# Optimization experiments

Measured on AMD Instinct MI355X. Metric: run time of the kernel, lower is better.

## Reference

```python
import jax, jax.numpy as jnp
import numpy as np

N = 50000  # nodes
E = 1600000  # edges
L = 2  # layers
D = 128  # input/hidden dim


def setup_inputs() -> dict:
    key = jax.random.key(0)
    ks = jax.random.split(key, 8)
    s = 1.0 / np.sqrt(D)
    return {
        "x": jax.random.normal(ks[0], (N, D), jnp.float32),
        "edge_index": jax.random.randint(ks[1], (2, E), 0, N, jnp.int64),
        "h": jax.random.normal(ks[2], (L, N, D), jnp.float32),
        "Wx": jax.random.normal(ks[3], (L, 3, D, D), jnp.float32) * s,
        "bx": jax.random.normal(ks[4], (L, 3, D), jnp.float32) * 0.01,
        "Wh": jax.random.normal(ks[5], (L, 3, D, D), jnp.float32) * s,
        "bh": jax.random.normal(ks[6], (L, 3, D), jnp.float32) * 0.01,
    }


def _gcn(x, W, b, src, dst, dinv):
    # GCNConv with added self-loops and symmetric normalization:
    # out = D^{-1/2} (A + I) D^{-1/2} X W + b
    hw = x @ W                                   # [N, H]
    norm = dinv[src] * dinv[dst]                 # [E]
    msg = hw[src] * norm[:, None]                # [E, H]
    agg = jax.ops.segment_sum(msg, dst, num_segments=N)
    agg = agg + hw * (dinv * dinv)[:, None]      # self-loop contribution
    return agg + b


def reference(x, edge_index, h, Wx, bx, Wh, bh):
    src = edge_index[0]
    dst = edge_index[1]
    # in-degree on destination nodes, including self-loop (+1)
    deg = jax.ops.segment_sum(jnp.ones((E,), x.dtype), dst, num_segments=N) + 1.0
    dinv = jax.lax.rsqrt(deg)

    outs = []
    inp = x
    for l in range(L):
        hl = h[l]
        z = jax.nn.sigmoid(_gcn(inp, Wx[l, 0], bx[l, 0], src, dst, dinv)
                           + _gcn(hl, Wh[l, 0], bh[l, 0], src, dst, dinv))
        r = jax.nn.sigmoid(_gcn(inp, Wx[l, 1], bx[l, 1], src, dst, dinv)
                           + _gcn(hl, Wh[l, 1], bh[l, 1], src, dst, dinv))
        h_tilde = jnp.tanh(_gcn(inp, Wx[l, 2], bx[l, 2], src, dst, dinv)
                           + _gcn(r * hl, Wh[l, 2], bh[l, 2], src, dst, dinv))
        out = z * hl + (1.0 - z) * h_tilde
        outs.append(out)
        inp = out
    return jnp.stack(outs, axis=0)  # [L, N, H]
```

## Files before the change

kernel.cpp:

```cpp
#include <hip/hip_runtime.h>

typedef __attribute__((ext_vector_type(8))) unsigned short us8;
typedef __attribute__((ext_vector_type(4))) unsigned short us4;
typedef __attribute__((ext_vector_type(8))) short s8;
typedef __attribute__((ext_vector_type(4))) float f4;
typedef __attribute__((ext_vector_type(2))) float f2;

#define DEV static __device__ __forceinline__
#define CAP 128
#define NRG 128
#define NBB 256
#define SEGC 128

DEV float bf2f(unsigned short h){ return __uint_as_float(((unsigned)h)<<16); }
DEV unsigned short f2bf(float f){
  unsigned x = __float_as_uint(f);
  x += 0x7fffu + ((x>>16)&1u);
  return (unsigned short)(x>>16);
}
DEV float sigm(float x){ return 1.f/(1.f + __expf(-x)); }

__global__ __launch_bounds__(256) void k_bucket(const int* __restrict__ src,
    const int* __restrict__ dst, unsigned* __restrict__ buf,
    int* __restrict__ cnt2, int e, int n){
  __shared__ int lcnt[NRG];
  int b = blockIdx.x;
  for(int i=threadIdx.x;i<NRG;i+=256) lcnt[i] = 0;
  __syncthreads();
  int chunk = (e + NBB - 1)/NBB;
  int lo = b*chunk;
  int hi = lo + chunk; if(hi>e) hi=e;
  for(int i = lo + threadIdx.x; i < hi; i += 256){
    int d = dst[i], s = src[i];
    int r = (d*NRG)/n;
    int pos = atomicAdd(&lcnt[r], 1);
    if(pos < SEGC)
      buf[((size_t)r*NBB + b)*SEGC + pos] = ((unsigned)d<<16) | (unsigned)s;
  }
  __syncthreads();
  for(int i=threadIdx.x;i<NRG;i+=256) cnt2[i*NBB + b] = lcnt[i];
}

__global__ __launch_bounds__(256) void k_build2(const unsigned* __restrict__ buf,
    const int* __restrict__ cnt2, int* __restrict__ cnt,
    unsigned short* __restrict__ col, int n){
  int r = blockIdx.x;
  int lo = (r*n + NRG-1)/NRG;
  int hi = ((r+1)*n + NRG-1)/NRG;
  int span = hi - lo;
  __shared__ int lc[512];
  for(int i=threadIdx.x; i<span; i+=256) lc[i] = 0;
  __syncthreads();
  int lane = threadIdx.x & 63;
  for(int seg = threadIdx.x>>6; seg < NBB; seg += 4){
    int c = cnt2[r*NBB + seg]; if(c > SEGC) c = SEGC;
    const unsigned* p = buf + ((size_t)r*NBB + seg)*SEGC;
    for(int i = lane; i < c; i += 64){
      unsigned v = p[i];
      int d = (int)(v >> 16), s = (int)(v & 0xffffu);
      int slot = atomicAdd(&lc[d - lo], 1);
      col[(size_t)d*CAP + slot] = (unsigned short)s;
    }
  }
  __syncthreads();
  for(int i=threadIdx.x; i<span; i+=256) cnt[lo + i] = lc[i];
}

__global__ void k_setup(const int* __restrict__ cnt, float* __restrict__ dinv, int n,
                        const float* __restrict__ Wx, const float* __restrict__ Wh,
                        unsigned short* __restrict__ WT,
                        const float* __restrict__ h, unsigned short* __restrict__ hb,
                        int htotal){
  int gN = (n + 255)/256;
  int b = blockIdx.x;
  if(b < gN){
    int i = b*256 + threadIdx.x;
    if(i<n) dinv[i] = rsqrtf((float)cnt[i] + 1.0f);
  } else if(b < gN + 768){
    int i = (b-gN)*256 + threadIdx.x;
    int m = i >> 15;
    int rem = i & 32767;
    int j = rem >> 8;
    int k = rem & 255;
    float v = (k<128) ? Wx[((size_t)m*128 + k)*128 + j]
                      : Wh[((size_t)m*128 + (k-128))*128 + j];
    WT[(size_t)m*32768 + j*256 + k] = f2bf(v);
  } else {
    size_t i = ((size_t)(b - gN - 768)*256 + threadIdx.x)*4;
    if(i < (size_t)htotal){
      f4 v = *(const f4*)(h + i);
      us4 w;
      #pragma unroll
      for(int j=0;j<4;++j) w[j] = f2bf(v[j]);
      *(us4*)(hb + i) = w;
    }
  }
}

__global__ void k_scale2(const float* __restrict__ inp, const unsigned short* __restrict__ hb0,
                         const float* __restrict__ dinv, unsigned char* __restrict__ y2, int n){
  int i = blockIdx.x*blockDim.x+threadIdx.x;
  if(i >= n*32) return;
  int node = i>>5, d0 = (i&31)*4;
  float dv = dinv[node];
  f4 a = *(const f4*)(inp + (size_t)node*128 + d0);
  us4 hv = *(const us4*)(hb0 + (size_t)node*128 + d0);
  unsigned pa = __builtin_amdgcn_cvt_pk_fp8_f32(dv*a[0], dv*a[1], 0, false);
  pa = __builtin_amdgcn_cvt_pk_fp8_f32(dv*a[2], dv*a[3], pa, true);
  unsigned pb = __builtin_amdgcn_cvt_pk_fp8_f32(dv*bf2f(hv[0]), dv*bf2f(hv[1]), 0, false);
  pb = __builtin_amdgcn_cvt_pk_fp8_f32(dv*bf2f(hv[2]), dv*bf2f(hv[3]), pb, true);
  *(unsigned*)(y2 + (size_t)node*256 + d0)       = pa;
  *(unsigned*)(y2 + (size_t)node*256 + 128 + d0) = pb;
}

template<int DB>
__global__ __launch_bounds__(256) void k_agg(const unsigned char* __restrict__ y,
    const int* __restrict__ cnt, const unsigned short* __restrict__ col,
    const float* __restrict__ dinv, unsigned short* __restrict__ out0, int n)
{
  constexpr int GL = DB/16;
  constexpr int NG = 64/GL;
  constexpr int U = 8;
  int tid = threadIdx.x;
  int wave = tid>>6, lane = tid&63;
  int g = lane/GL, gl = lane%GL;
  int node = blockIdx.x*(4*NG) + wave*NG + g;
  if(node >= n) return;
  const unsigned char* yb = y + (size_t)gl*16;
  float acc[16];
  {
    uint4 q = *(const uint4*)(yb + (size_t)node*DB);
    const unsigned* qw = (const unsigned*)&q;
    #pragma unroll
    for(int w=0;w<4;++w){
      f2 lo = __builtin_amdgcn_cvt_pk_f32_fp8(qw[w], false);
      f2 hi = __builtin_amdgcn_cvt_pk_f32_fp8(qw[w], true);
      acc[w*4+0]=lo[0]; acc[w*4+1]=lo[1]; acc[w*4+2]=hi[0]; acc[w*4+3]=hi[1];
    }
  }
  const unsigned short* myrow = col + (size_t)node*CAP;
  int c_ = cnt[node];
  int last = c_ - 1;
  for(int i=0; i<c_; i += U){
    int s[U];
    #pragma unroll
    for(int u=0;u<U;++u){
      int ii = i + u; ii = (ii < last) ? ii : last;
      s[u] = myrow[ii];
    }
    uint4 v[U];
    #pragma unroll
    for(int u=0;u<U;++u) v[u] = *(const uint4*)(yb + (size_t)s[u]*DB);
    #pragma unroll
    for(int u=0;u<U;++u){
      if(i + u < c_){
        const unsigned* qw = (const unsigned*)&v[u];
        #pragma unroll
        for(int w=0;w<4;++w){
          f2 lo = __builtin_amdgcn_cvt_pk_f32_fp8(qw[w], false);
          f2 hi = __builtin_amdgcn_cvt_pk_f32_fp8(qw[w], true);
          acc[w*4+0]+=lo[0]; acc[w*4+1]+=lo[1]; acc[w*4+2]+=hi[0]; acc[w*4+3]+=hi[1];
        }
      }
    }
  }
  float dv = dinv[node];
  us8 w0, w1;
  #pragma unroll
  for(int j=0;j<8;++j){ w0[j]=f2bf(acc[j]*dv); w1[j]=f2bf(acc[8+j]*dv); }
  int c = gl*16;
  *(us8*)(out0 + (size_t)node*DB + c)     = w0;
  *(us8*)(out0 + (size_t)node*DB + c + 8) = w1;
}

template<int KB>
DEV void stageB512(unsigned char* Bs, const unsigned short* Bsrc, int srcOff, int t){
  constexpr int CPR = KB/8;
  #pragma unroll
  for(int i=0;i<128*CPR/512;++i){
    int c = t + i*512;
    int j = c / CPR, kc = c % CPR;
    us8 v = *(const us8*)(Bsrc + (size_t)j*256 + srcOff + kc*8);
    *(us8*)(Bs + ((j*(KB*2) + kc*16) ^ ((j&7)<<4))) = v;
  }
}
template<int NK>
DEV void loadB(const unsigned short* A, int astride, int node, int nrows, int hi,
               s8 (&b)[NK]){
  const unsigned short* Ap = A + (size_t)(node < nrows ? node : 0)*astride + hi*8;
  #pragma unroll
  for(int kk=0;kk<NK;++kk) b[kk] = *(const s8*)(Ap + kk*32);
}
template<int KB, int NK, int NA>
DEV void mfmaW(const unsigned char* Bs, const s8 (&b)[NA], int lo, int hi,
               f4 (&acc)[8]){
  static_assert(NK <= NA, "not enough B fragments");
  #pragma unroll
  for(int kk=0;kk<NK;++kk){
    #pragma unroll
    for(int n=0;n<8;++n){
      int j = n*16+lo;
      s8 a = *(const s8*)(Bs + ((j*(KB*2) + kk*64 + hi*16) ^ ((lo&7)<<4)));
      acc[n] = __builtin_amdgcn_mfma_f32_16x16x32_bf16(a, b[kk], acc[n], 0,0,0);
    }
  }
}

__global__ __launch_bounds__(512) void k_gemmRH(
    const unsigned short* __restrict__ axah, const unsigned short* __restrict__ Wr,
    const unsigned short* __restrict__ Wh2, const unsigned short* __restrict__ hbl,
    const float* __restrict__ dinv, const float* __restrict__ bxr,
    const float* __restrict__ bhr, unsigned char* __restrict__ yq,
    unsigned short* __restrict__ Zbh, int nrows)
{
  __shared__ unsigned char Bs[65536];
  const int t = threadIdx.x, lane = t & 63, lo = lane & 15, hi = lane >> 4;
  const int node = blockIdx.x*128 + (t>>6)*16 + lo;
  const bool ok = node < nrows;
  s8 b256[8];
  loadB<8>(axah, 256, node, nrows, hi, b256);
  stageB512<256>(Bs, Wr, 0, t);
  f4 acc[8];
  #pragma unroll
  for(int n=0;n<8;++n) acc[n]=(f4)0.f;
  __syncthreads();
  mfmaW<256,8,8>(Bs, b256, lo, hi, acc);
  if(ok){
    float dv = dinv[node];
    const size_t base = (size_t)node*128;
    #pragma unroll
    for(int n=0;n<8;++n){
      int j0 = n*16 + hi*4;
      f4 b1v = *(const f4*)(bxr + j0);
      f4 b2v = *(const f4*)(bhr + j0);
      us4 hv = *(const us4*)(hbl + base + j0);
      float q0 = dv * sigm(acc[n][0] + b1v[0] + b2v[0]) * bf2f(hv[0]);
      float q1 = dv * sigm(acc[n][1] + b1v[1] + b2v[1]) * bf2f(hv[1]);
      float q2 = dv * sigm(acc[n][2] + b1v[2] + b2v[2]) * bf2f(hv[2]);
      float q3 = dv * sigm(acc[n][3] + b1v[3] + b2v[3]) * bf2f(hv[3]);
      unsigned pk = __builtin_amdgcn_cvt_pk_fp8_f32(q0, q1, 0, false);
      pk = __builtin_amdgcn_cvt_pk_fp8_f32(q2, q3, pk, true);
      *(unsigned*)(yq + base + j0) = pk;
    }
  }
  __syncthreads();
  stageB512<128>(Bs, Wh2, 0, t);
  f4 accH[8];
  #pragma unroll
  for(int n=0;n<8;++n) accH[n]=(f4)0.f;
  __syncthreads();
  mfmaW<128,4,8>(Bs, b256, lo, hi, accH);
  if(ok){
    const size_t base = (size_t)node*128;
    #pragma unroll
    for(int n=0;n<8;++n){
      int j0 = n*16 + hi*4;
      us4 w;
      #pragma unroll
      for(int tt=0;tt<4;++tt) w[tt] = f2bf(accH[n][tt]);
      *(us4*)(Zbh + base + j0) = w;
    }
  }
}

__global__ __launch_bounds__(512) void k_gemmZF(
    const unsigned short* __restrict__ axah, const unsigned short* __restrict__ aq,
    const unsigned short* __restrict__ Wz, const unsigned short* __restrict__ Wh2,
    const unsigned short* __restrict__ Zbh, const unsigned short* __restrict__ hbl,
    const unsigned short* __restrict__ hbn, const float* __restrict__ dinv,
    const float* __restrict__ bxz, const float* __restrict__ bhz,
    const float* __restrict__ bxh, const float* __restrict__ bhh,
    float* __restrict__ outp, unsigned char* __restrict__ y2out, int nrows)
{
  __shared__ unsigned char Bs[65536];
  const int t = threadIdx.x, lane = t & 63, lo = lane & 15, hi = lane >> 4;
  const int node = blockIdx.x*128 + (t>>6)*16 + lo;
  const bool ok = node < nrows;
  s8 b256[8], bq[4];
  loadB<8>(axah, 256, node, nrows, hi, b256);
  loadB<4>(aq, 128, node, nrows, hi, bq);
  stageB512<256>(Bs, Wz, 0, t);
  f4 accZ[8];
  #pragma unroll
  for(int n=0;n<8;++n) accZ[n]=(f4)0.f;
  __syncthreads();
  mfmaW<256,8,8>(Bs, b256, lo, hi, accZ);
  __syncthreads();
  stageB512<128>(Bs, Wh2, 128, t);
  f4 accH[8];
  #pragma unroll
  for(int n=0;n<8;++n) accH[n]=(f4)0.f;
  __syncthreads();
  mfmaW<128,4,4>(Bs, bq, lo, hi, accH);
  if(ok){
    float dv = dinv[node];
    const size_t base = (size_t)node*128;
    #pragma unroll
    for(int n=0;n<8;++n){
      int j0 = n*16 + hi*4;
      f4 bz1 = *(const f4*)(bxz + j0);
      f4 bz2 = *(const f4*)(bhz + j0);
      f4 bh1 = *(const f4*)(bxh + j0);
      f4 bh2 = *(const f4*)(bhh + j0);
      us4 zb = *(const us4*)(Zbh + base + j0);
      us4 hv = *(const us4*)(hbl + base + j0);
      f4 o;
      #pragma unroll
      for(int tt=0;tt<4;++tt){
        float z  = sigm(accZ[n][tt] + bz1[tt] + bz2[tt]);
        float ht = tanhf(accH[n][tt] + bf2f(zb[tt]) + bh1[tt] + bh2[tt]);
        o[tt] = z*bf2f(hv[tt]) + (1.f - z)*ht;
      }
      *(f4*)(outp + base + j0) = o;
      if(y2out){
        unsigned pk = __builtin_amdgcn_cvt_pk_fp8_f32(dv*o[0], dv*o[1], 0, false);
        pk = __builtin_amdgcn_cvt_pk_fp8_f32(dv*o[2], dv*o[3], pk, true);
        *(unsigned*)(y2out + (size_t)node*256 + j0) = pk;
        us4 hn = *(const us4*)(hbn + base + j0);
        unsigned ph = __builtin_amdgcn_cvt_pk_fp8_f32(dv*bf2f(hn[0]), dv*bf2f(hn[1]), 0, false);
        ph = __builtin_amdgcn_cvt_pk_fp8_f32(dv*bf2f(hn[2]), dv*bf2f(hn[3]), ph, true);
        *(unsigned*)(y2out + (size_t)node*256 + 128 + j0) = ph;
      }
    }
  }
}

extern "C" void kernel_launch(void* const* d_in, const int* in_sizes, int n_in,
                              void* d_out, int out_size, void* d_ws, size_t ws_size,
                              hipStream_t stream){
  const float* x  = (const float*)d_in[0];
  const int*   ei = (const int*)d_in[1];
  const float* h  = (const float*)d_in[2];
  const float* Wx = (const float*)d_in[3];
  const float* bx = (const float*)d_in[4];
  const float* Wh = (const float*)d_in[5];
  const float* bh = (const float*)d_in[6];
  float* out = (float*)d_out;

  const int N = in_sizes[0] / 128;
  const int E = in_sizes[1] / 2;
  const int L = in_sizes[2] / in_sizes[0];
  const int* src = ei;
  const int* dst = ei + E;

  char* w = (char*)d_ws;
  auto alloc = [&](size_t b)->char*{ char* p = w; w += (b + 255) & ~(size_t)255; return p; };
  int* cnt = (int*)alloc((size_t)N*sizeof(int));
  unsigned short* col = (unsigned short*)alloc((size_t)N*CAP*sizeof(short));
  float* dinv = (float*)alloc((size_t)N*sizeof(float));
  unsigned short* WT = (unsigned short*)alloc((size_t)6*32768*sizeof(short));
  unsigned short* hb = (unsigned short*)alloc((size_t)L*N*128*sizeof(short));
  unsigned char* y2 = (unsigned char*)alloc((size_t)N*256);
  unsigned short* axah = (unsigned short*)alloc((size_t)N*256*sizeof(short));
  unsigned char* yq = (unsigned char*)alloc((size_t)N*128);
  unsigned short* aq = (unsigned short*)alloc((size_t)N*128*sizeof(short));
  unsigned short* Zbh = (unsigned short*)alloc((size_t)N*128*sizeof(short));
  unsigned* ebuf = (unsigned*)alloc((size_t)NRG*NBB*SEGC*sizeof(unsigned));
  int* cnt2 = (int*)alloc((size_t)NRG*NBB*sizeof(int));

  const int gN = (N + 255)/256;
  const int gew = (N*32 + 255)/256;
  const int g128 = (N + 127)/128;
  const int gagg4 = (N + 15)/16;
  const int gagg2 = (N + 31)/32;
  const int htotal = L*N*128;
  const int ghb = (htotal + 1023)/1024;

  k_bucket<<<NBB,256,0,stream>>>(src, dst, ebuf, cnt2, E, N);
  k_build2<<<NRG,256,0,stream>>>(ebuf, cnt2, cnt, col, N);
  k_setup<<<gN + 768 + ghb,256,0,stream>>>(cnt, dinv, N, Wx, Wh, WT, h, hb, htotal);

  for(int l=0; l<L; ++l){
    const unsigned short* hbl = hb + (size_t)l*N*128;
    const float* bxz = bx + (size_t)(l*3+0)*128; const float* bhz = bh + (size_t)(l*3+0)*128;
    const float* bxr = bx + (size_t)(l*3+1)*128; const float* bhr = bh + (size_t)(l*3+1)*128;
    const float* bxh = bx + (size_t)(l*3+2)*128; const float* bhh = bh + (size_t)(l*3+2)*128;
    const unsigned short* Wz = WT + (size_t)(l*3+0)*32768;
    const unsigned short* Wr = WT + (size_t)(l*3+1)*32768;
    const unsigned short* Wh2= WT + (size_t)(l*3+2)*32768;

    if(l==0) k_scale2<<<gew,256,0,stream>>>(x, hbl, dinv, y2, N);
    k_agg<256><<<gagg4,256,0,stream>>>(y2, cnt, col, dinv, axah, N);
    k_gemmRH<<<g128,512,0,stream>>>(axah, Wr, Wh2, hbl, dinv, bxr, bhr, yq, Zbh, N);
    k_agg<128><<<gagg2,256,0,stream>>>(yq, cnt, col, dinv, aq, N);
    k_gemmZF<<<g128,512,0,stream>>>(axah, aq, Wz, Wh2, Zbh, hbl,
        (l+1<L) ? (hb + (size_t)(l+1)*N*128) : nullptr, dinv,
        bxz, bhz, bxh, bhh, out + (size_t)l*N*128,
        (l+1<L) ? y2 : nullptr, N);
  }
}
```

Baseline: 364.1 us.

## Split GEMM output columns across two blocks and fold scale kernel into setup

The two gate GEMM kernels now launch twice as many blocks, each computing half of the 128 output columns. Both weight slices are staged into shared memory at once, which removes the intermediate sync-and-restage step and cuts LDS use from 64KB to 48KB. Separately, the layer-0 fp8 scaling kernel is merged into the setup kernel, reading fp32 h directly and computing dinv inline, which saves one launch. The cost is that each node's input fragments are now loaded twice, once per column half.

```diff
diff --git a/kernel.cpp b/kernel.cpp
--- a/kernel.cpp
+++ b/kernel.cpp
@@ -70,8 +70,10 @@
                         const float* __restrict__ Wx, const float* __restrict__ Wh,
                         unsigned short* __restrict__ WT,
                         const float* __restrict__ h, unsigned short* __restrict__ hb,
-                        int htotal){
+                        int htotal, const float* __restrict__ x,
+                        unsigned char* __restrict__ y2){
   int gN = (n + 255)/256;
+  int ghb = (htotal + 1023)/1024;
   int b = blockIdx.x;
   if(b < gN){
     int i = b*256 + threadIdx.x;
@@ -85,7 +87,7 @@
     float v = (k<128) ? Wx[((size_t)m*128 + k)*128 + j]
                       : Wh[((size_t)m*128 + (k-128))*128 + j];
     WT[(size_t)m*32768 + j*256 + k] = f2bf(v);
-  } else {
+  } else if(b < gN + 768 + ghb){
     size_t i = ((size_t)(b - gN - 768)*256 + threadIdx.x)*4;
     if(i < (size_t)htotal){
       f4 v = *(const f4*)(h + i);
@@ -94,23 +96,21 @@
       for(int j=0;j<4;++j) w[j] = f2bf(v[j]);
       *(us4*)(hb + i) = w;
     }
-  }
-}
-
-__global__ void k_scale2(const float* __restrict__ inp, const unsigned short* __restrict__ hb0,
-                         const float* __restrict__ dinv, unsigned char* __restrict__ y2, int n){
-  int i = blockIdx.x*blockDim.x+threadIdx.x;
-  if(i >= n*32) return;
-  int node = i>>5, d0 = (i&31)*4;
-  float dv = dinv[node];
-  f4 a = *(const f4*)(inp + (size_t)node*128 + d0);
-  us4 hv = *(const us4*)(hb0 + (size_t)node*128 + d0);
-  unsigned pa = __builtin_amdgcn_cvt_pk_fp8_f32(dv*a[0], dv*a[1], 0, false);
-  pa = __builtin_amdgcn_cvt_pk_fp8_f32(dv*a[2], dv*a[3], pa, true);
-  unsigned pb = __builtin_amdgcn_cvt_pk_fp8_f32(dv*bf2f(hv[0]), dv*bf2f(hv[1]), 0, false);
-  pb = __builtin_amdgcn_cvt_pk_fp8_f32(dv*bf2f(hv[2]), dv*bf2f(hv[3]), pb, true);
-  *(unsigned*)(y2 + (size_t)node*256 + d0)       = pa;
-  *(unsigned*)(y2 + (size_t)node*256 + 128 + d0) = pb;
+  } else {
+    int i = (b - gN - 768 - ghb)*256 + threadIdx.x;
+    if(i < n*32){
+      int node = i>>5, d0 = (i&31)*4;
+      float dv = rsqrtf((float)cnt[node] + 1.0f);
+      f4 a = *(const f4*)(x + (size_t)node*128 + d0);
+      f4 hv = *(const f4*)(h + (size_t)node*128 + d0);
+      unsigned pa = __builtin_amdgcn_cvt_pk_fp8_f32(dv*a[0], dv*a[1], 0, false);
+      pa = __builtin_amdgcn_cvt_pk_fp8_f32(dv*a[2], dv*a[3], pa, true);
+      unsigned pb = __builtin_amdgcn_cvt_pk_fp8_f32(dv*hv[0], dv*hv[1], 0, false);
+      pb = __builtin_amdgcn_cvt_pk_fp8_f32(dv*hv[2], dv*hv[3], pb, true);
+      *(unsigned*)(y2 + (size_t)node*256 + d0)       = pa;
+      *(unsigned*)(y2 + (size_t)node*256 + 128 + d0) = pb;
+    }
+  }
 }
 
 template<int DB>
@@ -173,15 +173,22 @@
   *(us8*)(out0 + (size_t)node*DB + c + 8) = w1;
 }
 
-template<int KB>
-DEV void stageB512(unsigned char* Bs, const unsigned short* Bsrc, int srcOff, int t){
-  constexpr int CPR = KB/8;
-  #pragma unroll
-  for(int i=0;i<128*CPR/512;++i){
+DEV void stageW256(unsigned char* Bs, const unsigned short* W, int jbase, int t){
+  #pragma unroll
+  for(int i=0;i<4;++i){
     int c = t + i*512;
-    int j = c / CPR, kc = c % CPR;
-    us8 v = *(const us8*)(Bsrc + (size_t)j*256 + srcOff + kc*8);
-    *(us8*)(Bs + ((j*(KB*2) + kc*16) ^ ((j&7)<<4))) = v;
+    int j = c >> 5, kc = c & 31;
+    us8 v = *(const us8*)(W + (size_t)(jbase + j)*256 + kc*8);
+    *(us8*)(Bs + ((j*512 + kc*16) ^ ((j&7)<<4))) = v;
+  }
+}
+DEV void stageW128(unsigned char* Bs2, const unsigned short* W, int jbase, int srcOff, int t){
+  #pragma unroll
+  for(int i=0;i<2;++i){
+    int c = t + i*512;
+    int j = c >> 4, kc = c & 15;
+    us8 v = *(const us8*)(W + (size_t)(jbase + j)*256 + srcOff + kc*8);
+    *(us8*)(Bs2 + ((j*256 + kc*16) ^ ((j&7)<<4))) = v;
   }
 }
 template<int NK>
@@ -192,13 +199,13 @@
   for(int kk=0;kk<NK;++kk) b[kk] = *(const s8*)(Ap + kk*32);
 }
 template<int KB, int NK, int NA>
-DEV void mfmaW(const unsigned char* Bs, const s8 (&b)[NA], int lo, int hi,
-               f4 (&acc)[8]){
+DEV void mfmaW4(const unsigned char* Bs, const s8 (&b)[NA], int lo, int hi,
+                f4 (&acc)[4]){
   static_assert(NK <= NA, "not enough B fragments");
   #pragma unroll
   for(int kk=0;kk<NK;++kk){
     #pragma unroll
-    for(int n=0;n<8;++n){
+    for(int n=0;n<4;++n){
       int j = n*16+lo;
       s8 a = *(const s8*)(Bs + ((j*(KB*2) + kk*64 + hi*16) ^ ((lo&7)<<4)));
       acc[n] = __builtin_amdgcn_mfma_f32_16x16x32_bf16(a, b[kk], acc[n], 0,0,0);
@@ -213,48 +220,38 @@
     const float* __restrict__ bhr, unsigned char* __restrict__ yq,
     unsigned short* __restrict__ Zbh, int nrows)
 {
-  __shared__ unsigned char Bs[65536];
+  __shared__ unsigned char Bs[49152];
   const int t = threadIdx.x, lane = t & 63, lo = lane & 15, hi = lane >> 4;
-  const int node = blockIdx.x*128 + (t>>6)*16 + lo;
+  const int jh = blockIdx.x & 1, nb = blockIdx.x >> 1;
+  const int jbase = jh*64;
+  const int node = nb*128 + (t>>6)*16 + lo;
   const bool ok = node < nrows;
   s8 b256[8];
   loadB<8>(axah, 256, node, nrows, hi, b256);
-  stageB512<256>(Bs, Wr, 0, t);
-  f4 acc[8];
-  #pragma unroll
-  for(int n=0;n<8;++n) acc[n]=(f4)0.f;
-  __syncthreads();
-  mfmaW<256,8,8>(Bs, b256, lo, hi, acc);
+  stageW256(Bs, Wr, jbase, t);
+  stageW128(Bs + 32768, Wh2, jbase, 0, t);
+  f4 accR[4], accH[4];
+  #pragma unroll
+  for(int n=0;n<4;++n){ accR[n]=(f4)0.f; accH[n]=(f4)0.f; }
+  __syncthreads();
+  mfmaW4<256,8,8>(Bs, b256, lo, hi, accR);
+  mfmaW4<128,4,8>(Bs + 32768, b256, lo, hi, accH);
   if(ok){
     float dv = dinv[node];
     const size_t base = (size_t)node*128;
     #pragma unroll
-    for(int n=0;n<8;++n){
-      int j0 = n*16 + hi*4;
+    for(int n=0;n<4;++n){
+      int j0 = jbase + n*16 + hi*4;
       f4 b1v = *(const f4*)(bxr + j0);
       f4 b2v = *(const f4*)(bhr + j0);
       us4 hv = *(const us4*)(hbl + base + j0);
-      float q0 = dv * sigm(acc[n][0] + b1v[0] + b2v[0]) * bf2f(hv[0]);
-      float q1 = dv * sigm(acc[n][1] + b1v[1] + b2v[1]) * bf2f(hv[1]);
-      float q2 = dv * sigm(acc[n][2] + b1v[2] + b2v[2]) * bf2f(hv[2]);
-      float q3 = dv * sigm(acc[n][3] + b1v[3] + b2v[3]) * bf2f(hv[3]);
+      float q0 = dv * sigm(accR[n][0] + b1v[0] + b2v[0]) * bf2f(hv[0]);
+      float q1 = dv * sigm(accR[n][1] + b1v[1] + b2v[1]) * bf2f(hv[1]);
+      float q2 = dv * sigm(accR[n][2] + b1v[2] + b2v[2]) * bf2f(hv[2]);
+      float q3 = dv * sigm(accR[n][3] + b1v[3] + b2v[3]) * bf2f(hv[3]);
       unsigned pk = __builtin_amdgcn_cvt_pk_fp8_f32(q0, q1, 0, false);
       pk = __builtin_amdgcn_cvt_pk_fp8_f32(q2, q3, pk, true);
       *(unsigned*)(yq + base + j0) = pk;
-    }
-  }
-  __syncthreads();
-  stageB512<128>(Bs, Wh2, 0, t);
-  f4 accH[8];
-  #pragma unroll
-  for(int n=0;n<8;++n) accH[n]=(f4)0.f;
-  __syncthreads();
-  mfmaW<128,4,8>(Bs, b256, lo, hi, accH);
-  if(ok){
-    const size_t base = (size_t)node*128;
-    #pragma unroll
-    for(int n=0;n<8;++n){
-      int j0 = n*16 + hi*4;
       us4 w;
       #pragma unroll
       for(int tt=0;tt<4;++tt) w[tt] = f2bf(accH[n][tt]);
@@ -272,32 +269,29 @@
     const float* __restrict__ bxh, const float* __restrict__ bhh,
     float* __restrict__ outp, unsigned char* __restrict__ y2out, int nrows)
 {
-  __shared__ unsigned char Bs[65536];
+  __shared__ unsigned char Bs[49152];
   const int t = threadIdx.x, lane = t & 63, lo = lane & 15, hi = lane >> 4;
-  const int node = blockIdx.x*128 + (t>>6)*16 + lo;
+  const int jh = blockIdx.x & 1, nb = blockIdx.x >> 1;
+  const int jbase = jh*64;
+  const int node = nb*128 + (t>>6)*16 + lo;
   const bool ok = node < nrows;
   s8 b256[8], bq[4];
   loadB<8>(axah, 256, node, nrows, hi, b256);
   loadB<4>(aq, 128, node, nrows, hi, bq);
-  stageB512<256>(Bs, Wz, 0, t);
-  f4 accZ[8];
-  #pragma unroll
-  for(int n=0;n<8;++n) accZ[n]=(f4)0.f;
-  __syncthreads();
-  mfmaW<256,8,8>(Bs, b256, lo, hi, accZ);
-  __syncthreads();
-  stageB512<128>(Bs, Wh2, 128, t);
-  f4 accH[8];
-  #pragma unroll
-  for(int n=0;n<8;++n) accH[n]=(f4)0.f;
-  __syncthreads();
-  mfmaW<128,4,4>(Bs, bq, lo, hi, accH);
+  stageW256(Bs, Wz, jbase, t);
+  stageW128(Bs + 32768, Wh2, jbase, 128, t);
+  f4 accZ[4], accH[4];
+  #pragma unroll
+  for(int n=0;n<4;++n){ accZ[n]=(f4)0.f; accH[n]=(f4)0.f; }
+  __syncthreads();
+  mfmaW4<256,8,8>(Bs, b256, lo, hi, accZ);
+  mfmaW4<128,4,4>(Bs + 32768, bq, lo, hi, accH);
   if(ok){
     float dv = dinv[node];
     const size_t base = (size_t)node*128;
     #pragma unroll
-    for(int n=0;n<8;++n){
-      int j0 = n*16 + hi*4;
+    for(int n=0;n<4;++n){
+      int j0 = jbase + n*16 + hi*4;
       f4 bz1 = *(const f4*)(bxz + j0);
       f4 bz2 = *(const f4*)(bhz + j0);
       f4 bh1 = *(const f4*)(bxh + j0);
@@ -360,7 +354,7 @@
 
   const int gN = (N + 255)/256;
   const int gew = (N*32 + 255)/256;
-  const int g128 = (N + 127)/128;
+  const int gzf = 2*((N + 127)/128);
   const int gagg4 = (N + 15)/16;
   const int gagg2 = (N + 31)/32;
   const int htotal = L*N*128;
@@ -368,7 +362,8 @@
 
   k_bucket<<<NBB,256,0,stream>>>(src, dst, ebuf, cnt2, E, N);
   k_build2<<<NRG,256,0,stream>>>(ebuf, cnt2, cnt, col, N);
-  k_setup<<<gN + 768 + ghb,256,0,stream>>>(cnt, dinv, N, Wx, Wh, WT, h, hb, htotal);
+  k_setup<<<gN + 768 + ghb + gew,256,0,stream>>>(cnt, dinv, N, Wx, Wh, WT,
+                                                 h, hb, htotal, x, y2);
 
   for(int l=0; l<L; ++l){
     const unsigned short* hbl = hb + (size_t)l*N*128;
@@ -379,11 +374,10 @@
     const unsigned short* Wr = WT + (size_t)(l*3+1)*32768;
     const unsigned short* Wh2= WT + (size_t)(l*3+2)*32768;
 
-    if(l==0) k_scale2<<<gew,256,0,stream>>>(x, hbl, dinv, y2, N);
     k_agg<256><<<gagg4,256,0,stream>>>(y2, cnt, col, dinv, axah, N);
-    k_gemmRH<<<g128,512,0,stream>>>(axah, Wr, Wh2, hbl, dinv, bxr, bhr, yq, Zbh, N);
+    k_gemmRH<<<gzf,512,0,stream>>>(axah, Wr, Wh2, hbl, dinv, bxr, bhr, yq, Zbh, N);
     k_agg<128><<<gagg2,256,0,stream>>>(yq, cnt, col, dinv, aq, N);
-    k_gemmZF<<<g128,512,0,stream>>>(axah, aq, Wz, Wh2, Zbh, hbl,
+    k_gemmZF<<<gzf,512,0,stream>>>(axah, aq, Wz, Wh2, Zbh, hbl,
         (l+1<L) ? (hb + (size_t)(l+1)*N*128) : nullptr, dinv,
         bxz, bhz, bxh, bhh, out + (size_t)l*N*128,
         (l+1<L) ? y2 : nullptr, N);
```

Result: slower. 381.3 us (+4.7%).
